# Optimization experiments

Measured on AMD Instinct MI355X. Metric: run time of the kernel, lower is better.

## Reference

```python
import jax, jax.numpy as jnp
import numpy as np

B, H, S, D = 2, 16, 2048, 64
MASK_NEG = 1e9


def setup_inputs() -> dict:
    key = jax.random.key(0)
    kq, kk, kv, km = jax.random.split(key, 4)
    Q = jax.random.normal(kq, (B, H, S, D), dtype=jnp.float32)
    K = jax.random.normal(kk, (B, H, S, D), dtype=jnp.float32)
    V = jax.random.normal(kv, (B, H, S, D), dtype=jnp.float32)
    # float 0/1 mask, broadcast over heads; 1 = masked-out position
    attn_mask = jax.random.randint(km, (B, 1, S, S), 0, 2).astype(jnp.float32)
    return {"Q": Q, "K": K, "V": V, "attn_mask": attn_mask}


def reference(Q, K, V, attn_mask):
    # scores: [B, H, S, S]
    attn_score = jnp.einsum('bhqd,bhkd->bhqk', Q, K)
    scale = jnp.sqrt(jnp.asarray(K.shape[-1], dtype=jnp.float32))
    attn_scale = attn_score / scale - MASK_NEG * attn_mask
    attn_prob = jax.nn.softmax(attn_scale, axis=-1)
    attn_out = jnp.einsum('bhqk,bhkd->bhqd', attn_prob, V)
    return attn_out
```

## Files before the change

kernel.cpp:

```cpp
#include <hip/hip_runtime.h>


#define S_LEN 2048
#define D_DIM 64
#define WPR   32
#define NIT   32

typedef __attribute__((ext_vector_type(8)))  short bf16x8;
typedef __attribute__((ext_vector_type(4)))  float f32x4;
typedef __attribute__((ext_vector_type(16))) float f32x16;
typedef unsigned uint2v __attribute__((ext_vector_type(2)));
typedef unsigned long long ull;

__device__ __forceinline__ f32x16 mfma32(bf16x8 a, bf16x8 b, f32x16 c) {
  return __builtin_amdgcn_mfma_f32_32x32x16_bf16(a, b, c, 0, 0, 0);
}
__device__ __forceinline__ f32x4 mfma16(bf16x8 a, bf16x8 b, f32x4 c) {
  return __builtin_amdgcn_mfma_f32_16x16x32_bf16(a, b, c, 0, 0, 0);
}
__device__ __forceinline__ unsigned short f2bf(float f) {
  unsigned u = __builtin_bit_cast(unsigned, f);
  unsigned r = u + 0x7FFFu + ((u >> 16) & 1u);
  return (unsigned short)(r >> 16);
}
__device__ __forceinline__ float bf2f(unsigned short s) {
  unsigned u = ((unsigned)s) << 16;
  return __builtin_bit_cast(float, u);
}
__device__ __forceinline__ unsigned packbf(float a, float b) {
  unsigned r;
  asm("v_cvt_pk_bf16_f32 %0, %1, %2" : "=v"(r) : "v"(a), "v"(b));
  return r;
}
__device__ __forceinline__ float fexp2(float x) {
#if __has_builtin(__builtin_amdgcn_exp2f)
  return __builtin_amdgcn_exp2f(x);
#else
  return exp2f(x);
#endif
}
__device__ __forceinline__ bool detect_bf16(const void* maskp) {
  const unsigned short* s = (const unsigned short*)maskp;
  unsigned short v = s[2 * (threadIdx.x & 63)];
  return __ballot(v == (unsigned short)0x3F80) != 0ull;
}
__device__ __forceinline__ int4 cvt_f8(const float* p) {
  float4 f0 = *(const float4*)p;
  float4 f1 = *(const float4*)(p + 4);
  int4 r;
  r.x = (int)packbf(f0.x, f0.y);
  r.y = (int)packbf(f0.z, f0.w);
  r.z = (int)packbf(f1.x, f1.y);
  r.w = (int)packbf(f1.z, f1.w);
  return r;
}
__device__ __forceinline__ void gl_lds16(const unsigned short* g, unsigned short* l) {
#if __has_builtin(__builtin_amdgcn_global_load_lds)
  __builtin_amdgcn_global_load_lds(
      (const __attribute__((address_space(1))) unsigned int*)g,
      (__attribute__((address_space(3))) unsigned int*)l, 16, 0, 0);
#else
  *(int4*)((char*)l + (threadIdx.x & 63) * 16) = *(const int4*)g;
#endif
}

#define C1 0.18033688011112042f
#define C2 1.4426950408889634e9f

#define SEG0 4096u
#define SEG1 2048u
#define SEG2 1024u
#define SEG3 2048u

__global__ __launch_bounds__(256) void prep_all(
    const void* __restrict__ M, const void* __restrict__ Kin,
    const void* __restrict__ Vin, const void* __restrict__ Qin,
    ull* __restrict__ bits, unsigned short* __restrict__ Kf,
    unsigned short* __restrict__ Vf, unsigned short* __restrict__ Qc) {
  __shared__ __align__(16) unsigned short T[64 * 72];
  const bool isb = detect_bf16(M);
  const unsigned bx = blockIdx.x;
  const int tid = threadIdx.x;

  if (bx < SEG0) {
    unsigned e0 = bx * 2048u + tid;
    #pragma unroll
    for (int j = 0; j < 8; ++j) {
      unsigned idx = e0 + (unsigned)j * 256u;
      bool on = isb ? (bf2f(((const unsigned short*)M)[idx]) > 0.5f)
                    : (((const float*)M)[idx] > 0.5f);
      ull bm = __ballot(on);
      if ((tid & 63) == 0) {
        unsigned c = idx & 2047u, r = (idx >> 11) & 2047u, bb = idx >> 22;
        bits[(((size_t)(bb * WPR + (c >> 6))) << 11) + r] = bm;
      }
    }
  } else if (bx < SEG0 + SEG1) {
    unsigned g = (bx - SEG0) * 256u + tid;
    unsigned lane = g & 63u, f = (g >> 6) & 7u, it = (g >> 9) & 31u, bh = g >> 14;
    unsigned t = f >> 2, dc = f & 3, hi = lane >> 5, l31 = lane & 31;
    size_t src = (size_t)bh * (S_LEN * D_DIM) +
                 (size_t)(it * 64 + t * 32 + l31) * D_DIM + dc * 16 + hi * 8;
    int4 out;
    if (isb) out = *(const int4*)((const unsigned short*)Kin + src);
    else     out = cvt_f8((const float*)Kin + src);
    *(int4*)&Kf[(size_t)g * 8] = out;
  } else if (bx < SEG0 + SEG1 + SEG2) {
    unsigned idx = bx - (SEG0 + SEG1);
    unsigned bh = idx >> 5, it = idx & 31u;
    {
      int k = tid >> 2, d0 = (tid & 3) * 16;
      size_t src = (size_t)bh * (S_LEN * D_DIM) + (size_t)(it * 64 + k) * D_DIM + d0;
      int4 a, c;
      if (isb) {
        const unsigned short* s = (const unsigned short*)Vin + src;
        a = *(const int4*)s; c = *(const int4*)(s + 8);
      } else {
        const float* s = (const float*)Vin + src;
        a = cvt_f8(s); c = cvt_f8(s + 8);
      }
      *(int4*)&T[k * 72 + d0] = a;
      *(int4*)&T[k * 72 + d0 + 8] = c;
    }
    __syncthreads();
    #pragma unroll
    for (int h = 0; h < 2; ++h) {
      int c = tid + h * 256;
      int lane = c & 63, f = c >> 6;
      int t = f >> 2, kc = (f >> 1) & 1, dt = f & 1;
      int hi = lane >> 5, l31 = lane & 31;
      unsigned short v[8];
      #pragma unroll
      for (int j = 0; j < 8; ++j)
        v[j] = T[(t * 32 + kc * 16 + hi * 8 + j) * 72 + dt * 32 + l31];
      *(int4*)&Vf[(((size_t)(bh * 32 + it)) * 8 + f) * 512 + lane * 8] = *(int4*)v;
    }
  } else {
    size_t i0 = ((size_t)(bx - (SEG0 + SEG1 + SEG2)) * 256 + tid) * 8;
    unsigned short v[8];
    if (isb) {
      *(int4*)v = *(const int4*)((const unsigned short*)Qin + i0);
      #pragma unroll
      for (int j = 0; j < 8; ++j) v[j] = f2bf(bf2f(v[j]) * C1);
    } else {
      const float* f = (const float*)Qin + i0;
      #pragma unroll
      for (int j = 0; j < 4; ++j)
        *((unsigned*)v + j) = packbf(f[2 * j] * C1, f[2 * j + 1] * C1);
    }
    *(int4*)&Qc[i0] = *(int4*)v;
  }
}

__global__ __launch_bounds__(256, 4) void attn_fast(
    const unsigned short* __restrict__ Qc, const unsigned short* __restrict__ Kf,
    const unsigned short* __restrict__ Vf, const ull* __restrict__ bits,
    const void* __restrict__ maskp, void* __restrict__ Op) {
  __shared__ __align__(16) unsigned short Stg[2][2][8][512];

  const bool isb = detect_bf16(maskp);
  const int tid  = threadIdx.x;
  const int wave = tid >> 6;
  const int lane = tid & 63;
  const int hi   = lane >> 5;
  const int l31  = lane & 31;
  const int g    = wave >> 1;
  const int rw   = wave & 1;
  const int id   = blockIdx.x;
  const int slot = id >> 3;
  const int bh   = (id & 7) * 4 + (slot & 3);
  const int qb   = slot >> 2;
  const int qbase = qb * 64 + rw * 32;
  const int b    = bh >> 4;
  const size_t base = (size_t)bh * S_LEN * D_DIM;
  const int xidx = ((lane ^ 32) & 63) * 4;

  bf16x8 qf[4];
  #pragma unroll
  for (int dc = 0; dc < 4; ++dc)
    qf[dc] = *(const bf16x8*)&Qc[base + (size_t)(qbase + l31) * D_DIM + dc * 16 + hi * 8];

  bf16x8 onesb;
  #pragma unroll
  for (int i = 0; i < 8; ++i) onesb[i] = (short)0x3F80;

  const unsigned short* Kw = Kf + (size_t)bh * 131072 + (size_t)(2 * rw) * 512 + lane * 8;
  const unsigned short* Vw = Vf + (size_t)bh * 131072 + (size_t)(2 * rw) * 512 + lane * 8;
  const int ks0 = g * 32;
  const size_t bitbase = ((size_t)(b * WPR) << 11) + (size_t)(qbase + l31);

  f32x16 acc_o[2];
  f32x16 acc_l;
  f32x16 zv;
  #pragma unroll
  for (int r = 0; r < 16; ++r) {
    acc_o[0][r] = 0.f; acc_o[1][r] = 0.f; acc_l[r] = 0.f; zv[r] = 0.f;
  }

  {
    const size_t so = (size_t)ks0 * 2048;
    gl_lds16(Kw + so,       &Stg[g][0][2 * rw][0]);
    gl_lds16(Kw + so + 512, &Stg[g][0][2 * rw + 1][0]);
    gl_lds16(Vw + so,       &Stg[g][0][4 + 2 * rw][0]);
    gl_lds16(Vw + so + 512, &Stg[g][0][4 + 2 * rw + 1][0]);
  }
  __syncthreads();

  ull wcur = 0;
  #pragma unroll 2
  for (int f = 0; f < 32; ++f) {
    const int cur = f & 1;
    if (f < 31) {
      const size_t so = (size_t)(ks0 + f + 1) * 2048;
      gl_lds16(Kw + so,       &Stg[g][cur ^ 1][2 * rw][0]);
      gl_lds16(Kw + so + 512, &Stg[g][cur ^ 1][2 * rw + 1][0]);
      gl_lds16(Vw + so,       &Stg[g][cur ^ 1][4 + 2 * rw][0]);
      gl_lds16(Vw + so + 512, &Stg[g][cur ^ 1][4 + 2 * rw + 1][0]);
    }
    if (!(f & 1)) wcur = bits[bitbase + ((size_t)(g * 16 + (f >> 1)) << 11)];

    bf16x8 ka[4];
    #pragma unroll
    for (int dc = 0; dc < 4; ++dc)
      ka[dc] = *(const bf16x8*)&Stg[g][cur][dc][lane * 8];
    __builtin_amdgcn_s_setprio(1);
    f32x16 sc = mfma32(ka[0], qf[0], zv);
    #pragma unroll
    for (int dc = 1; dc < 4; ++dc) sc = mfma32(ka[dc], qf[dc], sc);
    __builtin_amdgcn_s_setprio(0);

    const unsigned wtv = (unsigned)((wcur >> (hi * 4)) >> (32 * (f & 1)));

    float p[16];
    #pragma unroll
    for (int r = 0; r < 16; ++r) {
      float e = fexp2(sc[r]);
      unsigned bit = (wtv >> ((r & 3) + 8 * (r >> 2))) & 1u;
      p[r] = bit ? 0.0f : e;
    }

    #pragma unroll
    for (int kc = 0; kc < 2; ++kc) {
      unsigned pk0 = packbf(p[8 * kc + 0], p[8 * kc + 1]);
      unsigned pk1 = packbf(p[8 * kc + 2], p[8 * kc + 3]);
      unsigned pk2 = packbf(p[8 * kc + 4], p[8 * kc + 5]);
      unsigned pk3 = packbf(p[8 * kc + 6], p[8 * kc + 7]);
      uint4 d;
#if __has_builtin(__builtin_amdgcn_permlane32_swap)
      uint2v s02 = __builtin_amdgcn_permlane32_swap(pk0, pk2, false, false);
      uint2v s13 = __builtin_amdgcn_permlane32_swap(pk1, pk3, false, false);
      d.x = s02[0]; d.z = s02[1];
      d.y = s13[0]; d.w = s13[1];
#else
      unsigned x0 = (unsigned)__builtin_amdgcn_ds_bpermute(xidx, (int)pk0);
      unsigned x1 = (unsigned)__builtin_amdgcn_ds_bpermute(xidx, (int)pk1);
      unsigned x2 = (unsigned)__builtin_amdgcn_ds_bpermute(xidx, (int)pk2);
      unsigned x3 = (unsigned)__builtin_amdgcn_ds_bpermute(xidx, (int)pk3);
      d.x = hi ? x2 : pk0;
      d.y = hi ? x3 : pk1;
      d.z = hi ? pk2 : x0;
      d.w = hi ? pk3 : x1;
#endif
      bf16x8 pf = __builtin_bit_cast(bf16x8, d);
      __builtin_amdgcn_s_setprio(1);
      #pragma unroll
      for (int dt = 0; dt < 2; ++dt) {
        bf16x8 vfr = *(const bf16x8*)&Stg[g][cur][4 + kc * 2 + dt][lane * 8];
        acc_o[dt] = mfma32(pf, vfr, acc_o[dt]);
      }
      acc_l = mfma32(pf, onesb, acc_l);
      __builtin_amdgcn_s_setprio(0);
    }

    __syncthreads();
  }

  float* Cb = (float*)Stg;
  if (g == 1) {
    #pragma unroll
    for (int r = 0; r < 16; ++r) {
      Cb[(rw * 48 + r) * 64 + lane]      = acc_o[0][r];
      Cb[(rw * 48 + 16 + r) * 64 + lane] = acc_o[1][r];
      Cb[(rw * 48 + 32 + r) * 64 + lane] = acc_l[r];
    }
  }
  __syncthreads();
  if (g == 0) {
    #pragma unroll
    for (int r = 0; r < 16; ++r) {
      float o0 = acc_o[0][r] + Cb[(rw * 48 + r) * 64 + lane];
      float o1 = acc_o[1][r] + Cb[(rw * 48 + 16 + r) * 64 + lane];
      float lv = acc_l[r]    + Cb[(rw * 48 + 32 + r) * 64 + lane];
      int m = (r & 3) + 8 * (r >> 2) + 4 * hi;
      float inv = 1.0f / lv;
      size_t idx = base + (size_t)(qbase + m) * D_DIM + l31;
      if (isb) {
        ((unsigned short*)Op)[idx]      = f2bf(o0 * inv);
        ((unsigned short*)Op)[idx + 32] = f2bf(o1 * inv);
      } else {
        ((float*)Op)[idx]      = o0 * inv;
        ((float*)Op)[idx + 32] = o1 * inv;
      }
    }
  }
}

__global__ __launch_bounds__(256, 2) void attn_fallback(
    const void* __restrict__ Qp, const void* __restrict__ Kp,
    const void* __restrict__ Vp, const void* __restrict__ maskp,
    void* __restrict__ Op) {
  __shared__ __align__(16) short QKlds[128 * 72];
  __shared__ __align__(16) short Vtlds[64 * 72];
  __shared__ __align__(16) short Plds2[128 * 72];

  const bool isb = detect_bf16(maskp);
  const int tid  = threadIdx.x;
  const int wave = tid >> 6;
  const int lane = tid & 63;
  const int l15  = lane & 15;
  const int quad = lane >> 4;
  const int q0   = blockIdx.x * 128;
  const int bh   = blockIdx.y;
  const int b    = bh >> 4;
  const size_t base = (size_t)bh * S_LEN * D_DIM;

  const short* Qs = (const short*)Qp; const float* Qf = (const float*)Qp;
  const short* Ks = (const short*)Kp; const float* Kf2 = (const float*)Kp;
  const short* Vs = (const short*)Vp; const float* Vf2 = (const float*)Vp;

  if (isb) {
    const short* Qg = Qs + base + (size_t)q0 * D_DIM;
    #pragma unroll
    for (int p = 0; p < 4; ++p) {
      int e = p * 2048 + tid * 8;
      *(int4*)&QKlds[(e >> 6) * 72 + (e & 63)] = *(const int4*)(Qg + e);
    }
  } else {
    const float* Qg = Qf + base + (size_t)q0 * D_DIM;
    #pragma unroll
    for (int p = 0; p < 4; ++p) {
      int e = p * 2048 + tid * 8;
      *(int4*)&QKlds[(e >> 6) * 72 + (e & 63)] = cvt_f8(Qg + e);
    }
  }
  __syncthreads();
  bf16x8 qf[2][2];
  #pragma unroll
  for (int mi = 0; mi < 2; ++mi)
    #pragma unroll
    for (int kt = 0; kt < 2; ++kt)
      qf[mi][kt] = *(const bf16x8*)&QKlds[(wave * 32 + mi * 16 + l15) * 72 + kt * 32 + quad * 8];
  __syncthreads();

  f32x4 acc_o[2][4];
  f32x4 acc_l[2];
  const f32x4 zero4 = {0.f, 0.f, 0.f, 0.f};
  #pragma unroll
  for (int mi = 0; mi < 2; ++mi) {
    acc_l[mi] = zero4;
    #pragma unroll
    for (int nt = 0; nt < 4; ++nt) acc_o[mi][nt] = zero4;
  }
  bf16x8 onesB;
  {
    short ov = (l15 == 0) ? (short)0x3F80 : (short)0;
    #pragma unroll
    for (int i = 0; i < 8; ++i) onesB[i] = ov;
  }

  for (int it = 0; it < NIT; ++it) {
    const int k0 = it * 64;
    if (isb) {
      const short* Kg = Ks + base + (size_t)k0 * D_DIM;
      #pragma unroll
      for (int p = 0; p < 2; ++p) {
        int e = p * 2048 + tid * 8;
        *(int4*)&QKlds[(e >> 6) * 72 + (e & 63)] = *(const int4*)(Kg + e);
      }
    } else {
      const float* Kg = Kf2 + base + (size_t)k0 * D_DIM;
      #pragma unroll
      for (int p = 0; p < 2; ++p) {
        int e = p * 2048 + tid * 8;
        *(int4*)&QKlds[(e >> 6) * 72 + (e & 63)] = cvt_f8(Kg + e);
      }
    }
    {
      const int r0 = (tid >> 3) * 2;
      const int d0 = (tid & 7) * 8;
      unsigned short as_[8], bs_[8];
      if (isb) {
        const short* Vg = Vs + base + (size_t)k0 * D_DIM;
        *(int4*)as_ = *(const int4*)(Vg + r0 * D_DIM + d0);
        *(int4*)bs_ = *(const int4*)(Vg + (r0 + 1) * D_DIM + d0);
      } else {
        const float* Vg = Vf2 + base + (size_t)k0 * D_DIM;
        *(int4*)as_ = cvt_f8(Vg + r0 * D_DIM + d0);
        *(int4*)bs_ = cvt_f8(Vg + (r0 + 1) * D_DIM + d0);
      }
      #pragma unroll
      for (int j = 0; j < 8; ++j) {
        int d = d0 + j;
        int blk = (r0 >> 3) ^ (d >> 3);
        unsigned pk = (unsigned)as_[j] | ((unsigned)bs_[j] << 16);
        *(unsigned*)&Vtlds[d * 72 + blk * 8 + (r0 & 7)] = pk;
      }
    }
    __syncthreads();

    f32x4 sc[2][4];
    #pragma unroll
    for (int mi = 0; mi < 2; ++mi)
      #pragma unroll
      for (int nt = 0; nt < 4; ++nt) sc[mi][nt] = zero4;
    #pragma unroll
    for (int nt = 0; nt < 4; ++nt) {
      bf16x8 kf0 = *(const bf16x8*)&QKlds[(nt * 16 + l15) * 72 + quad * 8];
      bf16x8 kf1 = *(const bf16x8*)&QKlds[(nt * 16 + l15) * 72 + 32 + quad * 8];
      #pragma unroll
      for (int mi = 0; mi < 2; ++mi) {
        sc[mi][nt] = mfma16(qf[mi][0], kf0, sc[mi][nt]);
        sc[mi][nt] = mfma16(qf[mi][1], kf1, sc[mi][nt]);
      }
    }

    #pragma unroll
    for (int mi = 0; mi < 2; ++mi) {
      #pragma unroll
      for (int nt = 0; nt < 4; ++nt) {
        #pragma unroll
        for (int reg = 0; reg < 4; ++reg) {
          int rg = q0 + wave * 32 + mi * 16 + quad * 4 + reg;
          size_t mix = (size_t)b * S_LEN * S_LEN + (size_t)rg * S_LEN + k0 + nt * 16 + l15;
          float mv = isb ? bf2f(((const unsigned short*)maskp)[mix])
                         : ((const float*)maskp)[mix];
          float y = sc[mi][nt][reg] * C1 - mv * C2;
          Plds2[(wave * 32 + mi * 16 + quad * 4 + reg) * 72 + nt * 16 + l15] =
              (short)f2bf(fexp2(y));
        }
      }
    }
    __syncthreads();

    #pragma unroll
    for (int kt = 0; kt < 2; ++kt) {
      bf16x8 pf[2];
      #pragma unroll
      for (int mi = 0; mi < 2; ++mi)
        pf[mi] = *(const bf16x8*)&Plds2[(wave * 32 + mi * 16 + l15) * 72 + kt * 32 + quad * 8];
      #pragma unroll
      for (int nt = 0; nt < 4; ++nt) {
        int d = nt * 16 + l15;
        int kb = (kt * 4 + quad) ^ (d >> 3);
        bf16x8 vf = *(const bf16x8*)&Vtlds[d * 72 + kb * 8];
        #pragma unroll
        for (int mi = 0; mi < 2; ++mi)
          acc_o[mi][nt] = mfma16(pf[mi], vf, acc_o[mi][nt]);
      }
      #pragma unroll
      for (int mi = 0; mi < 2; ++mi)
        acc_l[mi] = mfma16(pf[mi], onesB, acc_l[mi]);
    }
    __syncthreads();
  }

  #pragma unroll
  for (int mi = 0; mi < 2; ++mi) {
    #pragma unroll
    for (int reg = 0; reg < 4; ++reg) {
      float lv = __shfl(acc_l[mi][reg], lane & 48, 64);
      float inv = 1.0f / lv;
      #pragma unroll
      for (int nt = 0; nt < 4; ++nt) {
        float o = acc_o[mi][nt][reg] * inv;
        size_t idx = base + (size_t)(q0 + wave * 32 + mi * 16 + quad * 4 + reg) * D_DIM + nt * 16 + l15;
        if (isb) ((unsigned short*)Op)[idx] = f2bf(o);
        else     ((float*)Op)[idx] = o;
      }
    }
  }
}

extern "C" void kernel_launch(void* const* d_in, const int* in_sizes, int n_in,
                              void* d_out, int out_size, void* d_ws, size_t ws_size,
                              hipStream_t stream) {
  const void* Q = d_in[0];
  const void* K = d_in[1];
  const void* V = d_in[2];
  const void* M = d_in[3];

  dim3 block(256);
  const size_t bits_bytes = (size_t)2 * S_LEN * S_LEN / 8;
  const size_t tens_bytes = (size_t)2 * 16 * S_LEN * D_DIM * 2;

  if (ws_size >= bits_bytes + 3 * tens_bytes) {
    char* ws = (char*)d_ws;
    ull* bits = (ull*)ws;
    unsigned short* Kf = (unsigned short*)(ws + bits_bytes);
    unsigned short* Vf = (unsigned short*)(ws + bits_bytes + tens_bytes);
    unsigned short* Qc = (unsigned short*)(ws + bits_bytes + 2 * tens_bytes);
    prep_all<<<dim3(SEG0 + SEG1 + SEG2 + SEG3), block, 0, stream>>>(
        M, K, V, Q, bits, Kf, Vf, Qc);
    attn_fast<<<dim3(1024), block, 0, stream>>>(Qc, Kf, Vf, bits, M, d_out);
  } else {
    attn_fallback<<<dim3(S_LEN / 128, 32), block, 0, stream>>>(Q, K, V, M, d_out);
  }
}
```

Baseline: 170.0 us.

## Triple-buffer K/V staging with two-deep prefetch and partial vmcnt waits

Moves the K/V LDS staging from a double buffer to a triple buffer, so each wave prefetches the tile two iterations ahead. Barriers now wait only until at most four loads are outstanding (vmcnt(4)) rather than draining all loads, which keeps the next tile's global-to-LDS copies in flight across the barrier. The larger LDS footprint forces the launch bound down from 4 to 3 blocks per CU, trading occupancy for deeper latency hiding. The correctness of the partial waits depends on the vmcnt count covering the loads for the tile about to be consumed, including the interleaved mask-bit loads.

Result: slower. 176.1 us (+3.6%).

```diff
diff --git a/kernel.cpp b/kernel.cpp
--- a/kernel.cpp
+++ b/kernel.cpp
@@ -152,11 +152,11 @@
   }
 }
 
-__global__ __launch_bounds__(256, 4) void attn_fast(
+__global__ __launch_bounds__(256, 3) void attn_fast(
     const unsigned short* __restrict__ Qc, const unsigned short* __restrict__ Kf,
     const unsigned short* __restrict__ Vf, const ull* __restrict__ bits,
     const void* __restrict__ maskp, void* __restrict__ Op) {
-  __shared__ __align__(16) unsigned short Stg[2][2][8][512];
+  __shared__ __align__(16) unsigned short Stg[2][3][8][512];
 
   const bool isb = detect_bf16(maskp);
   const int tid  = threadIdx.x;
@@ -197,27 +197,31 @@
     acc_o[0][r] = 0.f; acc_o[1][r] = 0.f; acc_l[r] = 0.f; zv[r] = 0.f;
   }
 
-  {
-    const size_t so = (size_t)ks0 * 2048;
-    gl_lds16(Kw + so,       &Stg[g][0][2 * rw][0]);
-    gl_lds16(Kw + so + 512, &Stg[g][0][2 * rw + 1][0]);
-    gl_lds16(Vw + so,       &Stg[g][0][4 + 2 * rw][0]);
-    gl_lds16(Vw + so + 512, &Stg[g][0][4 + 2 * rw + 1][0]);
-  }
-  __syncthreads();
+  #pragma unroll
+  for (int s = 0; s < 2; ++s) {
+    const size_t so = (size_t)(ks0 + s) * 2048;
+    gl_lds16(Kw + so,       &Stg[g][s][2 * rw][0]);
+    gl_lds16(Kw + so + 512, &Stg[g][s][2 * rw + 1][0]);
+    gl_lds16(Vw + so,       &Stg[g][s][4 + 2 * rw][0]);
+    gl_lds16(Vw + so + 512, &Stg[g][s][4 + 2 * rw + 1][0]);
+  }
+  asm volatile("s_waitcnt vmcnt(4)" ::: "memory");
+  __builtin_amdgcn_sched_barrier(0);
+  __builtin_amdgcn_s_barrier();
+  __builtin_amdgcn_sched_barrier(0);
 
   ull wcur = 0;
-  #pragma unroll 2
+  int cur = 0;
   for (int f = 0; f < 32; ++f) {
-    const int cur = f & 1;
-    if (f < 31) {
-      const size_t so = (size_t)(ks0 + f + 1) * 2048;
-      gl_lds16(Kw + so,       &Stg[g][cur ^ 1][2 * rw][0]);
-      gl_lds16(Kw + so + 512, &Stg[g][cur ^ 1][2 * rw + 1][0]);
-      gl_lds16(Vw + so,       &Stg[g][cur ^ 1][4 + 2 * rw][0]);
-      gl_lds16(Vw + so + 512, &Stg[g][cur ^ 1][4 + 2 * rw + 1][0]);
-    }
     if (!(f & 1)) wcur = bits[bitbase + ((size_t)(g * 16 + (f >> 1)) << 11)];
+    if (f < 30) {
+      int nb = cur + 2; if (nb >= 3) nb -= 3;
+      const size_t so = (size_t)(ks0 + f + 2) * 2048;
+      gl_lds16(Kw + so,       &Stg[g][nb][2 * rw][0]);
+      gl_lds16(Kw + so + 512, &Stg[g][nb][2 * rw + 1][0]);
+      gl_lds16(Vw + so,       &Stg[g][nb][4 + 2 * rw][0]);
+      gl_lds16(Vw + so + 512, &Stg[g][nb][4 + 2 * rw + 1][0]);
+    }
 
     bf16x8 ka[4];
     #pragma unroll
@@ -272,9 +276,15 @@
       __builtin_amdgcn_s_setprio(0);
     }
 
-    __syncthreads();
-  }
-
+    if (f < 30) asm volatile("s_waitcnt vmcnt(4)" ::: "memory");
+    else        asm volatile("s_waitcnt vmcnt(0)" ::: "memory");
+    __builtin_amdgcn_sched_barrier(0);
+    __builtin_amdgcn_s_barrier();
+    __builtin_amdgcn_sched_barrier(0);
+    cur = (cur == 2) ? 0 : cur + 1;
+  }
+
+  __syncthreads();
   float* Cb = (float*)Stg;
   if (g == 1) {
     #pragma unroll
```

## Pre-transpose mask bits into wave masks and skip bf16 K/Q prep copies

Applied to the files above, without the earlier changes.

Adds a prep_w kernel that uses ballots to rewrite the mask bit array in place into per-row 64-bit lane masks. The attention loop can then read one scalar mask per score register and select with v_cndmask, replacing per-element shift-and-test work. For bf16 inputs the K and Q prep segments now exit early: attention scales Q inline and reads K directly from the raw tensor with a different stride. This adds a kernel launch and many more scalar mask loads per iteration, and the test inputs are float32, so the bf16 paths do not run.

New measurement: 170.9 us. About the same (+0.6%).

```diff
diff --git a/kernel.cpp b/kernel.cpp
--- a/kernel.cpp
+++ b/kernel.cpp
@@ -96,15 +96,13 @@
       }
     }
   } else if (bx < SEG0 + SEG1) {
+    if (isb) return;
     unsigned g = (bx - SEG0) * 256u + tid;
     unsigned lane = g & 63u, f = (g >> 6) & 7u, it = (g >> 9) & 31u, bh = g >> 14;
     unsigned t = f >> 2, dc = f & 3, hi = lane >> 5, l31 = lane & 31;
     size_t src = (size_t)bh * (S_LEN * D_DIM) +
                  (size_t)(it * 64 + t * 32 + l31) * D_DIM + dc * 16 + hi * 8;
-    int4 out;
-    if (isb) out = *(const int4*)((const unsigned short*)Kin + src);
-    else     out = cvt_f8((const float*)Kin + src);
-    *(int4*)&Kf[(size_t)g * 8] = out;
+    *(int4*)&Kf[(size_t)g * 8] = cvt_f8((const float*)Kin + src);
   } else if (bx < SEG0 + SEG1 + SEG2) {
     unsigned idx = bx - (SEG0 + SEG1);
     unsigned bh = idx >> 5, it = idx & 31u;
@@ -136,25 +134,41 @@
       *(int4*)&Vf[(((size_t)(bh * 32 + it)) * 8 + f) * 512 + lane * 8] = *(int4*)v;
     }
   } else {
+    if (isb) return;
     size_t i0 = ((size_t)(bx - (SEG0 + SEG1 + SEG2)) * 256 + tid) * 8;
     unsigned short v[8];
-    if (isb) {
-      *(int4*)v = *(const int4*)((const unsigned short*)Qin + i0);
-      #pragma unroll
-      for (int j = 0; j < 8; ++j) v[j] = f2bf(bf2f(v[j]) * C1);
-    } else {
-      const float* f = (const float*)Qin + i0;
-      #pragma unroll
-      for (int j = 0; j < 4; ++j)
-        *((unsigned*)v + j) = packbf(f[2 * j] * C1, f[2 * j + 1] * C1);
-    }
+    const float* f = (const float*)Qin + i0;
+    #pragma unroll
+    for (int j = 0; j < 4; ++j)
+      *((unsigned*)v + j) = packbf(f[2 * j] * C1, f[2 * j + 1] * C1);
     *(int4*)&Qc[i0] = *(int4*)v;
   }
 }
 
+__global__ __launch_bounds__(256) void prep_w(ull* __restrict__ bits) {
+  const int tid = threadIdx.x;
+  const int wave = tid >> 6;
+  const int lane = tid & 63;
+  const int hi = lane >> 5;
+  const unsigned uid = blockIdx.x * 4 + wave;
+  const unsigned b = uid >> 11, w = (uid >> 6) & 31u, q32 = uid & 63u;
+  ull* base = bits + (((size_t)(b * 32 + w)) << 11) + (size_t)q32 * 32;
+  const ull wc = base[lane & 31];
+  #pragma unroll
+  for (int sub = 0; sub < 2; ++sub) {
+    #pragma unroll
+    for (int r = 0; r < 16; ++r) {
+      int pos = sub * 32 + (r & 3) + 8 * (r >> 2) + 4 * hi;
+      ull W = __ballot(((wc >> pos) & 1ull) != 0ull);
+      if (lane == 0) base[sub * 16 + r] = W;
+    }
+  }
+}
+
 __global__ __launch_bounds__(256, 4) void attn_fast(
-    const unsigned short* __restrict__ Qc, const unsigned short* __restrict__ Kf,
-    const unsigned short* __restrict__ Vf, const ull* __restrict__ bits,
+    const unsigned short* __restrict__ Qc, const void* __restrict__ Qraw,
+    const unsigned short* __restrict__ Kf, const void* __restrict__ Kraw,
+    const unsigned short* __restrict__ Vf, const ull* __restrict__ Wm,
     const void* __restrict__ maskp, void* __restrict__ Op) {
   __shared__ __align__(16) unsigned short Stg[2][2][8][512];
 
@@ -164,8 +178,9 @@
   const int lane = tid & 63;
   const int hi   = lane >> 5;
   const int l31  = lane & 31;
-  const int g    = wave >> 1;
-  const int rw   = wave & 1;
+  const int wvu  = __builtin_amdgcn_readfirstlane(wave);
+  const int g    = wvu >> 1;
+  const int rw   = wvu & 1;
   const int id   = blockIdx.x;
   const int slot = id >> 3;
   const int bh   = (id & 7) * 4 + (slot & 3);
@@ -176,18 +191,39 @@
   const int xidx = ((lane ^ 32) & 63) * 4;
 
   bf16x8 qf[4];
-  #pragma unroll
-  for (int dc = 0; dc < 4; ++dc)
-    qf[dc] = *(const bf16x8*)&Qc[base + (size_t)(qbase + l31) * D_DIM + dc * 16 + hi * 8];
+  if (isb) {
+    #pragma unroll
+    for (int dc = 0; dc < 4; ++dc) {
+      bf16x8 q = *(const bf16x8*)((const unsigned short*)Qraw + base +
+                    (size_t)(qbase + l31) * D_DIM + dc * 16 + hi * 8);
+      #pragma unroll
+      for (int j = 0; j < 8; ++j)
+        q[j] = (short)f2bf(bf2f((unsigned short)q[j]) * C1);
+      qf[dc] = q;
+    }
+  } else {
+    #pragma unroll
+    for (int dc = 0; dc < 4; ++dc)
+      qf[dc] = *(const bf16x8*)&Qc[base + (size_t)(qbase + l31) * D_DIM + dc * 16 + hi * 8];
+  }
 
   bf16x8 onesb;
   #pragma unroll
   for (int i = 0; i < 8; ++i) onesb[i] = (short)0x3F80;
 
-  const unsigned short* Kw = Kf + (size_t)bh * 131072 + (size_t)(2 * rw) * 512 + lane * 8;
+  const unsigned short* Kw0;
+  size_t kd;
+  if (isb) {
+    Kw0 = (const unsigned short*)Kraw + base + (size_t)l31 * D_DIM + (2 * rw) * 16 + hi * 8;
+    kd = 16;
+  } else {
+    Kw0 = Kf + (size_t)bh * 131072 + (size_t)(2 * rw) * 512 + lane * 8;
+    kd = 512;
+  }
   const unsigned short* Vw = Vf + (size_t)bh * 131072 + (size_t)(2 * rw) * 512 + lane * 8;
   const int ks0 = g * 32;
-  const size_t bitbase = ((size_t)(b * WPR) << 11) + (size_t)(qbase + l31);
+
+  const ull* WmU = Wm + (((size_t)(b * 32)) << 11) + (size_t)(qb * 2 + rw) * 32;
 
   f32x16 acc_o[2];
   f32x16 acc_l;
@@ -199,25 +235,25 @@
 
   {
     const size_t so = (size_t)ks0 * 2048;
-    gl_lds16(Kw + so,       &Stg[g][0][2 * rw][0]);
-    gl_lds16(Kw + so + 512, &Stg[g][0][2 * rw + 1][0]);
+    gl_lds16(Kw0 + so,      &Stg[g][0][2 * rw][0]);
+    gl_lds16(Kw0 + so + kd, &Stg[g][0][2 * rw + 1][0]);
     gl_lds16(Vw + so,       &Stg[g][0][4 + 2 * rw][0]);
     gl_lds16(Vw + so + 512, &Stg[g][0][4 + 2 * rw + 1][0]);
   }
   __syncthreads();
 
-  ull wcur = 0;
   #pragma unroll 2
   for (int f = 0; f < 32; ++f) {
     const int cur = f & 1;
     if (f < 31) {
       const size_t so = (size_t)(ks0 + f + 1) * 2048;
-      gl_lds16(Kw + so,       &Stg[g][cur ^ 1][2 * rw][0]);
-      gl_lds16(Kw + so + 512, &Stg[g][cur ^ 1][2 * rw + 1][0]);
+      gl_lds16(Kw0 + so,      &Stg[g][cur ^ 1][2 * rw][0]);
+      gl_lds16(Kw0 + so + kd, &Stg[g][cur ^ 1][2 * rw + 1][0]);
       gl_lds16(Vw + so,       &Stg[g][cur ^ 1][4 + 2 * rw][0]);
       gl_lds16(Vw + so + 512, &Stg[g][cur ^ 1][4 + 2 * rw + 1][0]);
     }
-    if (!(f & 1)) wcur = bits[bitbase + ((size_t)(g * 16 + (f >> 1)) << 11)];
+    const int ks = ks0 + f;
+    const ull* Wp = WmU + (((size_t)(ks >> 1)) << 11) + (size_t)(ks & 1) * 16;
 
     bf16x8 ka[4];
     #pragma unroll
@@ -229,14 +265,12 @@
     for (int dc = 1; dc < 4; ++dc) sc = mfma32(ka[dc], qf[dc], sc);
     __builtin_amdgcn_s_setprio(0);
 
-    const unsigned wtv = (unsigned)((wcur >> (hi * 4)) >> (32 * (f & 1)));
-
     float p[16];
     #pragma unroll
     for (int r = 0; r < 16; ++r) {
       float e = fexp2(sc[r]);
-      unsigned bit = (wtv >> ((r & 3) + 8 * (r >> 2))) & 1u;
-      p[r] = bit ? 0.0f : e;
+      ull mr = Wp[r];
+      asm("v_cndmask_b32 %0, %1, 0, %2" : "=v"(p[r]) : "v"(e), "s"(mr));
     }
 
     #pragma unroll
@@ -501,7 +535,8 @@
     unsigned short* Qc = (unsigned short*)(ws + bits_bytes + 2 * tens_bytes);
     prep_all<<<dim3(SEG0 + SEG1 + SEG2 + SEG3), block, 0, stream>>>(
         M, K, V, Q, bits, Kf, Vf, Qc);
-    attn_fast<<<dim3(1024), block, 0, stream>>>(Qc, Kf, Vf, bits, M, d_out);
+    prep_w<<<dim3(1024), block, 0, stream>>>(bits);
+    attn_fast<<<dim3(1024), block, 0, stream>>>(Qc, Q, Kf, K, Vf, bits, M, d_out);
   } else {
     attn_fallback<<<dim3(S_LEN / 128, 32), block, 0, stream>>>(Q, K, V, M, d_out);
   }
```
